# Performance work log

Hardware: AMD Instinct MI355X
Metric: run time of the kernel (lower is better)

The kernel has to match this reference:

```python
import jax, jax.numpy as jnp
import numpy as np

B, S, D, H = 2, 2048, 1024, 16
HD = D // H
FF = 4 * D
EPS = 1e-5


def _ln(x, g, b):
    mu = jnp.mean(x, axis=-1, keepdims=True)
    var = jnp.var(x, axis=-1, keepdims=True)
    return (x - mu) * jax.lax.rsqrt(var + EPS) * g + b


def setup_inputs() -> dict:
    key = jax.random.key(0)
    ks = jax.random.split(key, 8)
    std = 0.02
    inp = {
        'x': jax.random.normal(ks[0], (B, S, D), jnp.float32),
        'mask': jnp.ones((B, S), jnp.int32),
        'Wq': jax.random.normal(ks[1], (D, D), jnp.float32) * std,
        'bq': jnp.zeros((D,), jnp.float32),
        'Wk': jax.random.normal(ks[2], (D, D), jnp.float32) * std,
        'bk': jnp.zeros((D,), jnp.float32),
        'Wv': jax.random.normal(ks[3], (D, D), jnp.float32) * std,
        'bv': jnp.zeros((D,), jnp.float32),
        'Wo': jax.random.normal(ks[4], (D, D), jnp.float32) * std,
        'bo': jnp.zeros((D,), jnp.float32),
        'W1': jax.random.normal(ks[5], (D, FF), jnp.float32) * std,
        'b1': jnp.zeros((FF,), jnp.float32),
        'W2': jax.random.normal(ks[6], (FF, D), jnp.float32) * std,
        'b2': jnp.zeros((D,), jnp.float32),
        'g1': jnp.ones((D,), jnp.float32),
        'be1': jnp.zeros((D,), jnp.float32),
        'g2': jnp.ones((D,), jnp.float32),
        'be2': jnp.zeros((D,), jnp.float32),
    }
    return inp


def reference(x, mask, Wq, bq, Wk, bk, Wv, bv, Wo, bo, W1, b1, W2, b2, g1, be1, g2, be2):
    # multi-head attention (dropout in eval mode => identity)
    q = (x @ Wq + bq).reshape(B, S, H, HD).transpose(0, 2, 1, 3)  # [B,H,S,HD]
    k = (x @ Wk + bk).reshape(B, S, H, HD).transpose(0, 2, 1, 3)
    v = (x @ Wv + bv).reshape(B, S, H, HD).transpose(0, 2, 1, 3)
    scores = jnp.einsum('bhqd,bhkd->bhqk', q, k) / jnp.sqrt(jnp.float32(HD))
    m = mask[:, None, None, :]  # [B,1,1,S] broadcast over queries
    scores = jnp.where(m == 0, jnp.float32(-1e9), scores)
    attn = jax.nn.softmax(scores, axis=-1)
    ao = jnp.einsum('bhqk,bhkd->bhqd', attn, v).transpose(0, 2, 1, 3).reshape(B, S, D)
    attn_out = ao @ Wo + bo
    x1 = _ln(x + attn_out, g1, be1)
    ffn = jax.nn.relu(x1 @ W1 + b1) @ W2 + b2
    return _ln(x1 + ffn, g2, be2)
```

## Files before the change

kernel.cpp:

```cpp
#include <hip/hip_runtime.h>
#include <stdint.h>
#include <stddef.h>

#define B_ 2
#define S_ 2048
#define D_ 1024
#define H_ 16
#define HD_ 64
#define FF_ 4096

typedef unsigned short u16;
typedef __attribute__((ext_vector_type(8))) short bf16x8;
typedef __attribute__((ext_vector_type(4))) float f32x4;

__device__ __forceinline__ u16 f2bf(float f) {
  unsigned u = __float_as_uint(f);
  u += 0x7fffu + ((u >> 16) & 1u);
  return (u16)(u >> 16);
}

__device__ __forceinline__ f32x4 mfma16(bf16x8 a, bf16x8 b, f32x4 c) {
  return __builtin_amdgcn_mfma_f32_16x16x32_bf16(a, b, c, 0, 0, 0);
}

__device__ __forceinline__ void gload16(const void* g, void* l) {
  __builtin_amdgcn_global_load_lds(
      (const __attribute__((address_space(1))) void*)g,
      (__attribute__((address_space(3))) void*)l, 16, 0, 0);
}

__global__ __launch_bounds__(256) void cvt_kernel(const float* __restrict__ src,
                                                  u16* __restrict__ dst, int n) {
  int i = (blockIdx.x * 256 + threadIdx.x) * 4;
  if (i >= n) return;
  float4 v = *(const float4*)(src + i);
  ushort4 o = { f2bf(v.x), f2bf(v.y), f2bf(v.z), f2bf(v.w) };
  *(ushort4*)(dst + i) = o;
}

__global__ __launch_bounds__(256) void transpose_cvt_kernel(
    const float* __restrict__ W, u16* __restrict__ WT, int K, int N) {
  __shared__ u16 t[32][33];
  int k0 = blockIdx.x * 32;
  int n0 = blockIdx.y * 32;
  int tid = threadIdx.x;
  int r = tid >> 3;
  int c = (tid & 7) << 2;
  float4 v = *(const float4*)(W + (size_t)(k0 + r) * N + n0 + c);
  t[r][c + 0] = f2bf(v.x); t[r][c + 1] = f2bf(v.y);
  t[r][c + 2] = f2bf(v.z); t[r][c + 3] = f2bf(v.w);
  __syncthreads();
  ushort4 o;
  o.x = t[c + 0][r]; o.y = t[c + 1][r]; o.z = t[c + 2][r]; o.w = t[c + 3][r];
  *(ushort4*)(WT + (size_t)(n0 + r) * K + k0 + c) = o;
}

template <int MODE>
__global__ __launch_bounds__(256) void gemm_bt(
    const u16* __restrict__ A, const u16* __restrict__ BT,
    const float* __restrict__ bias, void* __restrict__ outp,
    int M, int N, int K) {
  __shared__ __align__(16) u16 As[128 * 32];
  __shared__ __align__(16) u16 Bs[128 * 32];
  int tid = threadIdx.x;
  int lane = tid & 63;
  int wave = tid >> 6;
  int quad = lane >> 4;
  int l16 = lane & 15;
  int m0 = blockIdx.x * 128;
  int n0 = blockIdx.y * 128;
  int wm = (wave >> 1) * 64;
  int wn = (wave & 1) * 64;

  f32x4 zero = {0.f, 0.f, 0.f, 0.f};
  f32x4 acc[4][4];
#pragma unroll
  for (int i = 0; i < 4; i++)
#pragma unroll
    for (int j = 0; j < 4; j++) acc[i][j] = zero;

  int c0 = tid, c1 = tid + 256;
  const u16* ga0 = A + (size_t)(m0 + (c0 >> 2)) * K + (c0 & 3) * 8;
  const u16* ga1 = A + (size_t)(m0 + (c1 >> 2)) * K + (c1 & 3) * 8;
  const u16* gb0 = BT + (size_t)(n0 + (c0 >> 2)) * K + (c0 & 3) * 8;
  const u16* gb1 = BT + (size_t)(n0 + (c1 >> 2)) * K + (c1 & 3) * 8;

  for (int k0 = 0; k0 < K; k0 += 32) {
    gload16(ga0 + k0, &As[c0 * 8]);
    gload16(ga1 + k0, &As[c1 * 8]);
    gload16(gb0 + k0, &Bs[c0 * 8]);
    gload16(gb1 + k0, &Bs[c1 * 8]);
    __syncthreads();
    bf16x8 af[4], bfr[4];
#pragma unroll
    for (int i = 0; i < 4; i++)
      af[i] = *(const bf16x8*)&As[(wm + i * 16 + l16) * 32 + quad * 8];
#pragma unroll
    for (int j = 0; j < 4; j++)
      bfr[j] = *(const bf16x8*)&Bs[(wn + j * 16 + l16) * 32 + quad * 8];
#pragma unroll
    for (int i = 0; i < 4; i++)
#pragma unroll
      for (int j = 0; j < 4; j++)
        acc[i][j] = mfma16(af[i], bfr[j], acc[i][j]);
    __syncthreads();
  }

#pragma unroll
  for (int j = 0; j < 4; j++) {
    int gcol = n0 + wn + j * 16 + l16;
    float bv = bias[gcol];
#pragma unroll
    for (int i = 0; i < 4; i++) {
#pragma unroll
      for (int r = 0; r < 4; r++) {
        int grow = m0 + wm + i * 16 + quad * 4 + r;
        float val = acc[i][j][r] + bv;
        ((u16*)outp)[(size_t)grow * N + gcol] = f2bf(val > 0.f ? val : 0.f);
      }
    }
  }
}

__global__ __launch_bounds__(256) void gemm_bt64(
    const u16* __restrict__ A, const u16* __restrict__ BT,
    const float* __restrict__ bias, float* __restrict__ outp,
    int M, int N, int K) {
  __shared__ __align__(16) u16 As[128 * 32];
  __shared__ __align__(16) u16 Bs[64 * 32];
  int tid = threadIdx.x;
  int lane = tid & 63;
  int wave = tid >> 6;
  int quad = lane >> 4;
  int l16 = lane & 15;
  int m0 = blockIdx.x * 128;
  int n0 = blockIdx.y * 64;
  int wm = (wave >> 1) * 64;
  int wn = (wave & 1) * 32;

  f32x4 zero = {0.f, 0.f, 0.f, 0.f};
  f32x4 acc[4][2];
#pragma unroll
  for (int i = 0; i < 4; i++)
#pragma unroll
    for (int j = 0; j < 2; j++) acc[i][j] = zero;

  int c0 = tid, c1 = tid + 256;
  const u16* ga0 = A + (size_t)(m0 + (c0 >> 2)) * K + (c0 & 3) * 8;
  const u16* ga1 = A + (size_t)(m0 + (c1 >> 2)) * K + (c1 & 3) * 8;
  const u16* gb0 = BT + (size_t)(n0 + (tid >> 2)) * K + (tid & 3) * 8;

  for (int k0 = 0; k0 < K; k0 += 32) {
    gload16(ga0 + k0, &As[c0 * 8]);
    gload16(ga1 + k0, &As[c1 * 8]);
    gload16(gb0 + k0, &Bs[tid * 8]);
    __syncthreads();
    bf16x8 af[4], bfr[2];
#pragma unroll
    for (int i = 0; i < 4; i++)
      af[i] = *(const bf16x8*)&As[(wm + i * 16 + l16) * 32 + quad * 8];
#pragma unroll
    for (int j = 0; j < 2; j++)
      bfr[j] = *(const bf16x8*)&Bs[(wn + j * 16 + l16) * 32 + quad * 8];
#pragma unroll
    for (int i = 0; i < 4; i++)
#pragma unroll
      for (int j = 0; j < 2; j++)
        acc[i][j] = mfma16(af[i], bfr[j], acc[i][j]);
    __syncthreads();
  }

#pragma unroll
  for (int j = 0; j < 2; j++) {
    int gcol = n0 + wn + j * 16 + l16;
    float bv = bias[gcol];
#pragma unroll
    for (int i = 0; i < 4; i++) {
#pragma unroll
      for (int r = 0; r < 4; r++) {
        int grow = m0 + wm + i * 16 + quad * 4 + r;
        outp[(size_t)grow * N + gcol] = acc[i][j][r] + bv;
      }
    }
  }
}

__global__ __launch_bounds__(256) void gemm_qkv(
    const u16* __restrict__ A, const u16* __restrict__ BT,
    const float* __restrict__ bq, const float* __restrict__ bk,
    const float* __restrict__ bvp,
    u16* __restrict__ qb, u16* __restrict__ kb, u16* __restrict__ vb) {
  const int K = 1024;
  __shared__ __align__(16) u16 As[128 * 32];
  __shared__ __align__(16) u16 Bs[128 * 32];
  int tid = threadIdx.x;
  int lane = tid & 63;
  int wave = tid >> 6;
  int quad = lane >> 4;
  int l16 = lane & 15;
  int m0 = blockIdx.x * 128;
  int n0 = blockIdx.y * 128;
  int wm = (wave >> 1) * 64;
  int wn = (wave & 1) * 64;

  f32x4 zero = {0.f, 0.f, 0.f, 0.f};
  f32x4 acc[4][4];
#pragma unroll
  for (int i = 0; i < 4; i++)
#pragma unroll
    for (int j = 0; j < 4; j++) acc[i][j] = zero;

  int c0 = tid, c1 = tid + 256;
  const u16* ga0 = A + (size_t)(m0 + (c0 >> 2)) * K + (c0 & 3) * 8;
  const u16* ga1 = A + (size_t)(m0 + (c1 >> 2)) * K + (c1 & 3) * 8;
  const u16* gb0 = BT + (size_t)(n0 + (c0 >> 2)) * K + (c0 & 3) * 8;
  const u16* gb1 = BT + (size_t)(n0 + (c1 >> 2)) * K + (c1 & 3) * 8;

  for (int k0 = 0; k0 < K; k0 += 32) {
    gload16(ga0 + k0, &As[c0 * 8]);
    gload16(ga1 + k0, &As[c1 * 8]);
    gload16(gb0 + k0, &Bs[c0 * 8]);
    gload16(gb1 + k0, &Bs[c1 * 8]);
    __syncthreads();
    bf16x8 af[4], bfr[4];
#pragma unroll
    for (int i = 0; i < 4; i++)
      af[i] = *(const bf16x8*)&As[(wm + i * 16 + l16) * 32 + quad * 8];
#pragma unroll
    for (int j = 0; j < 4; j++)
      bfr[j] = *(const bf16x8*)&Bs[(wn + j * 16 + l16) * 32 + quad * 8];
#pragma unroll
    for (int i = 0; i < 4; i++)
#pragma unroll
      for (int j = 0; j < 4; j++)
        acc[i][j] = mfma16(af[i], bfr[j], acc[i][j]);
    __syncthreads();
  }

  int region = n0 >> 10;
  const float* bias = region == 0 ? bq : (region == 1 ? bk : bvp);
  u16* outp = region == 0 ? qb : (region == 1 ? kb : vb);

#pragma unroll
  for (int j = 0; j < 4; j++) {
    int gcol = (n0 & 1023) + wn + j * 16 + l16;
    float bv = bias[gcol];
    int h = gcol >> 6, hd = gcol & 63;
#pragma unroll
    for (int i = 0; i < 4; i++) {
#pragma unroll
      for (int r = 0; r < 4; r++) {
        int grow = m0 + wm + i * 16 + quad * 4 + r;
        float val = acc[i][j][r] + bv;
        int b = grow >> 11, s = grow & 2047;
        if (region < 2) {
          outp[(((size_t)(b * H_ + h)) * S_ + s) * HD_ + hd] = f2bf(val);
        } else {
          outp[(((size_t)(b * H_ + h)) * HD_ + hd) * S_ + s] = f2bf(val);
        }
      }
    }
  }
}

__global__ __launch_bounds__(256, 4) void attn_kernel(
    const u16* __restrict__ q, const u16* __restrict__ k,
    const u16* __restrict__ vt, const int* __restrict__ mask,
    u16* __restrict__ ao) {
  __shared__ __align__(16) u16 Ks[64 * 72];
  __shared__ __align__(16) u16 Vs[64 * 72];
  __shared__ __align__(16) u16 Ps[4][16 * 72];
  int tid = threadIdx.x;
  int lane = tid & 63;
  int wave = tid >> 6;
  int quad = lane >> 4;
  int l16 = lane & 15;
  int bh = blockIdx.y;
  int b = bh >> 4;
  int h = bh & 15;
  int qrow0 = blockIdx.x * 64 + wave * 16;

  const u16* qh = q + (size_t)bh * S_ * HD_;
  const u16* kh = k + (size_t)bh * S_ * HD_;
  const u16* vh = vt + (size_t)bh * HD_ * S_;

  bf16x8 qf0 = *(const bf16x8*)(qh + (size_t)(qrow0 + l16) * HD_ + quad * 8);
  bf16x8 qf1 = *(const bf16x8*)(qh + (size_t)(qrow0 + l16) * HD_ + 32 + quad * 8);

  int sr = tid >> 3, sc = tid & 7;
  const u16* kg0 = kh + sr * HD_ + sc * 8;
  const u16* kg1 = kh + (sr + 32) * HD_ + sc * 8;
  const u16* vg0 = vh + (size_t)sr * S_ + sc * 8;
  const u16* vg1 = vh + (size_t)(sr + 32) * S_ + sc * 8;
  int so0 = sr * 72 + sc * 8;
  int so1 = (sr + 32) * 72 + sc * 8;
  const int* mrow = mask + b * S_ + l16;

  float l_part[4] = {0.f, 0.f, 0.f, 0.f};
  f32x4 zero = {0.f, 0.f, 0.f, 0.f};
  f32x4 o_acc[4];
#pragma unroll
  for (int c = 0; c < 4; c++) o_acc[c] = zero;

  u16* pw = &Ps[wave][0];
  const float cexp = 0.125f * 1.4426950408889634f;

  for (int kt = 0; kt < S_; kt += 64) {
    bf16x8 kv0 = *(const bf16x8*)(kg0 + (size_t)kt * HD_);
    bf16x8 kv1 = *(const bf16x8*)(kg1 + (size_t)kt * HD_);
    bf16x8 vv0 = *(const bf16x8*)(vg0 + kt);
    bf16x8 vv1 = *(const bf16x8*)(vg1 + kt);
    int mks[4];
#pragma unroll
    for (int kg = 0; kg < 4; kg++) mks[kg] = mrow[kt + kg * 16];

    __syncthreads();
    *(bf16x8*)&Ks[so0] = kv0;
    *(bf16x8*)&Ks[so1] = kv1;
    *(bf16x8*)&Vs[so0] = vv0;
    *(bf16x8*)&Vs[so1] = vv1;
    __syncthreads();

    f32x4 s[4];
#pragma unroll
    for (int kg = 0; kg < 4; kg++) {
      bf16x8 kb0 = *(const bf16x8*)&Ks[(kg * 16 + l16) * 72 + quad * 8];
      bf16x8 kb1 = *(const bf16x8*)&Ks[(kg * 16 + l16) * 72 + 32 + quad * 8];
      f32x4 t0 = mfma16(qf0, kb0, zero);
      s[kg] = mfma16(qf1, kb1, t0);
    }
#pragma unroll
    for (int kg = 0; kg < 4; kg++) {
#pragma unroll
      for (int r = 0; r < 4; r++) {
        float e = exp2f(s[kg][r] * cexp);
        float p = mks[kg] ? e : 0.f;
        l_part[r] += p;
        pw[(quad * 4 + r) * 72 + kg * 16 + l16] = f2bf(p);
      }
    }
    bf16x8 pf0 = *(const bf16x8*)&pw[l16 * 72 + quad * 8];
    bf16x8 pf1 = *(const bf16x8*)&pw[l16 * 72 + 32 + quad * 8];
#pragma unroll
    for (int c = 0; c < 4; c++) {
      bf16x8 vf0 = *(const bf16x8*)&Vs[(c * 16 + l16) * 72 + quad * 8];
      bf16x8 vf1 = *(const bf16x8*)&Vs[(c * 16 + l16) * 72 + 32 + quad * 8];
      o_acc[c] = mfma16(pf0, vf0, o_acc[c]);
      o_acc[c] = mfma16(pf1, vf1, o_acc[c]);
    }
  }

#pragma unroll
  for (int r = 0; r < 4; r++) {
    float s = l_part[r];
#pragma unroll
    for (int off = 1; off < 16; off <<= 1) s += __shfl_xor(s, off);
    float inv = 1.f / s;
    int srow = qrow0 + quad * 4 + r;
#pragma unroll
    for (int c = 0; c < 4; c++) {
      float val = o_acc[c][r] * inv;
      ao[((size_t)(b * S_ + srow)) * D_ + h * HD_ + c * 16 + l16] = f2bf(val);
    }
  }
}

__global__ __launch_bounds__(256) void ln_kernel(
    const float* __restrict__ xa, const float* __restrict__ xadd,
    const float* __restrict__ g, const float* __restrict__ be,
    float* __restrict__ outf, u16* __restrict__ outb) {
  int row = blockIdx.x;
  int tid = threadIdx.x;
  int lane = tid & 63;
  int wv = tid >> 6;
  const float4 a = *(const float4*)(xa + (size_t)row * D_ + tid * 4);
  const float4 c = *(const float4*)(xadd + (size_t)row * D_ + tid * 4);
  float v0 = a.x + c.x, v1 = a.y + c.y, v2 = a.z + c.z, v3 = a.w + c.w;
  float s = v0 + v1 + v2 + v3;
  float sq = v0 * v0 + v1 * v1 + v2 * v2 + v3 * v3;
#pragma unroll
  for (int off = 1; off < 64; off <<= 1) {
    s += __shfl_xor(s, off);
    sq += __shfl_xor(sq, off);
  }
  __shared__ float red[8];
  if (lane == 0) { red[wv] = s; red[4 + wv] = sq; }
  __syncthreads();
  s = red[0] + red[1] + red[2] + red[3];
  sq = red[4] + red[5] + red[6] + red[7];
  float mean = s * (1.f / D_);
  float var = sq * (1.f / D_) - mean * mean;
  float rstd = rsqrtf(var + 1e-5f);
  const float4 gv = *(const float4*)(g + tid * 4);
  const float4 bv = *(const float4*)(be + tid * 4);
  float y0 = (v0 - mean) * rstd * gv.x + bv.x;
  float y1 = (v1 - mean) * rstd * gv.y + bv.y;
  float y2 = (v2 - mean) * rstd * gv.z + bv.z;
  float y3 = (v3 - mean) * rstd * gv.w + bv.w;
  float4 o = {y0, y1, y2, y3};
  *(float4*)(outf + (size_t)row * D_ + tid * 4) = o;
  if (outb) {
    ushort4 ob = {f2bf(y0), f2bf(y1), f2bf(y2), f2bf(y3)};
    *(ushort4*)(outb + (size_t)row * D_ + tid * 4) = ob;
  }
}

extern "C" void kernel_launch(void* const* d_in, const int* in_sizes, int n_in,
                              void* d_out, int out_size, void* d_ws, size_t ws_size,
                              hipStream_t stream) {
  const float* x = (const float*)d_in[0];
  const int* mask = (const int*)d_in[1];
  const float* Wq = (const float*)d_in[2];
  const float* bq = (const float*)d_in[3];
  const float* Wk = (const float*)d_in[4];
  const float* bk = (const float*)d_in[5];
  const float* Wv = (const float*)d_in[6];
  const float* bv = (const float*)d_in[7];
  const float* Wo = (const float*)d_in[8];
  const float* bo = (const float*)d_in[9];
  const float* W1 = (const float*)d_in[10];
  const float* b1 = (const float*)d_in[11];
  const float* W2 = (const float*)d_in[12];
  const float* b2 = (const float*)d_in[13];
  const float* g1 = (const float*)d_in[14];
  const float* be1 = (const float*)d_in[15];
  const float* g2 = (const float*)d_in[16];
  const float* be2 = (const float*)d_in[17];

  const size_t MB = 1ull << 20;
  char* ws = (char*)d_ws;
  u16* wTq = (u16*)(ws + 0 * MB);
  u16* wTk = (u16*)(ws + 2 * MB);
  u16* wTv = (u16*)(ws + 4 * MB);
  u16* wTo = (u16*)(ws + 6 * MB);
  u16* w1T = (u16*)(ws + 8 * MB);
  u16* w2T = (u16*)(ws + 16 * MB);
  u16* xb  = (u16*)(ws + 24 * MB);
  u16* qb  = (u16*)(ws + 32 * MB);
  u16* kb  = (u16*)(ws + 40 * MB);
  u16* vb  = (u16*)(ws + 48 * MB);
  u16* ao  = (u16*)(ws + 56 * MB);
  float* proj = (float*)(ws + 64 * MB);
  float* x1f  = (float*)(ws + 24 * MB);
  u16*   x1b  = (u16*)(ws + 40 * MB);
  u16*   h1   = (u16*)(ws + 48 * MB);
  float* ffn2 = (float*)(ws + 80 * MB);

  cvt_kernel<<<dim3((B_ * S_ * D_) / 1024), dim3(256), 0, stream>>>(x, xb, B_ * S_ * D_);
  transpose_cvt_kernel<<<dim3(32, 32), dim3(256), 0, stream>>>(Wq, wTq, D_, D_);
  transpose_cvt_kernel<<<dim3(32, 32), dim3(256), 0, stream>>>(Wk, wTk, D_, D_);
  transpose_cvt_kernel<<<dim3(32, 32), dim3(256), 0, stream>>>(Wv, wTv, D_, D_);
  transpose_cvt_kernel<<<dim3(32, 32), dim3(256), 0, stream>>>(Wo, wTo, D_, D_);
  transpose_cvt_kernel<<<dim3(32, 128), dim3(256), 0, stream>>>(W1, w1T, D_, FF_);
  transpose_cvt_kernel<<<dim3(128, 32), dim3(256), 0, stream>>>(W2, w2T, FF_, D_);

  gemm_qkv<<<dim3(32, 24), dim3(256), 0, stream>>>(xb, wTq, bq, bk, bv, qb, kb, vb);

  attn_kernel<<<dim3(S_ / 64, B_ * H_), dim3(256), 0, stream>>>(qb, kb, vb, mask, ao);

  gemm_bt64<<<dim3(32, 16), dim3(256), 0, stream>>>(ao, wTo, bo, proj, 4096, 1024, 1024);

  ln_kernel<<<dim3(4096), dim3(256), 0, stream>>>(x, proj, g1, be1, x1f, x1b);

  gemm_bt<3><<<dim3(32, 32), dim3(256), 0, stream>>>(x1b, w1T, b1, h1, 4096, 4096, 1024);
  gemm_bt64<<<dim3(32, 16), dim3(256), 0, stream>>>(h1, w2T, b2, ffn2, 4096, 1024, 4096);

  ln_kernel<<<dim3(4096), dim3(256), 0, stream>>>(x1f, ffn2, g2, be2, (float*)d_out, (u16*)nullptr);
}
```

Before: 431.8 us.

## Use split-K 128x128 GEMMs for output projections, fold softmax scale into Q

The Wo and W2 GEMMs change from 128x64 tiles to 128x128 tiles with a 2-way split-K. Each half writes its own fp32 partial buffer, and the LayerNorm kernel sums both partials with the residual. This raises data reuse per tile while keeping the block count, in exchange for more fp32 partial-buffer traffic. The softmax scale times log2(e) is now applied in the QKV epilogue, so the attention loop skips a per-element multiply. Attention also permutes the K rows in shared memory so that two adjacent probabilities can be packed into one 32-bit store, and the mask is read as int2.

```diff
diff --git a/kernel.cpp b/kernel.cpp
--- a/kernel.cpp
+++ b/kernel.cpp
@@ -55,10 +55,9 @@
   *(ushort4*)(WT + (size_t)(n0 + r) * K + k0 + c) = o;
 }
 
-template <int MODE>
-__global__ __launch_bounds__(256) void gemm_bt(
+__global__ __launch_bounds__(256) void gemm_bt_relu(
     const u16* __restrict__ A, const u16* __restrict__ BT,
-    const float* __restrict__ bias, void* __restrict__ outp,
+    const float* __restrict__ bias, u16* __restrict__ outp,
     int M, int N, int K) {
   __shared__ __align__(16) u16 As[128 * 32];
   __shared__ __align__(16) u16 Bs[128 * 32];
@@ -116,70 +115,75 @@
       for (int r = 0; r < 4; r++) {
         int grow = m0 + wm + i * 16 + quad * 4 + r;
         float val = acc[i][j][r] + bv;
-        ((u16*)outp)[(size_t)grow * N + gcol] = f2bf(val > 0.f ? val : 0.f);
-      }
-    }
-  }
-}
-
-__global__ __launch_bounds__(256) void gemm_bt64(
+        outp[(size_t)grow * N + gcol] = f2bf(val > 0.f ? val : 0.f);
+      }
+    }
+  }
+}
+
+__global__ __launch_bounds__(256) void gemm_bt_sk2(
     const u16* __restrict__ A, const u16* __restrict__ BT,
     const float* __restrict__ bias, float* __restrict__ outp,
-    int M, int N, int K) {
+    int M, int N, int K, int Kc) {
   __shared__ __align__(16) u16 As[128 * 32];
-  __shared__ __align__(16) u16 Bs[64 * 32];
+  __shared__ __align__(16) u16 Bs[128 * 32];
   int tid = threadIdx.x;
   int lane = tid & 63;
   int wave = tid >> 6;
   int quad = lane >> 4;
   int l16 = lane & 15;
   int m0 = blockIdx.x * 128;
-  int n0 = blockIdx.y * 64;
+  int n0 = blockIdx.y * 128;
+  int kb = blockIdx.z * Kc;
   int wm = (wave >> 1) * 64;
-  int wn = (wave & 1) * 32;
+  int wn = (wave & 1) * 64;
 
   f32x4 zero = {0.f, 0.f, 0.f, 0.f};
-  f32x4 acc[4][2];
+  f32x4 acc[4][4];
 #pragma unroll
   for (int i = 0; i < 4; i++)
 #pragma unroll
-    for (int j = 0; j < 2; j++) acc[i][j] = zero;
+    for (int j = 0; j < 4; j++) acc[i][j] = zero;
 
   int c0 = tid, c1 = tid + 256;
-  const u16* ga0 = A + (size_t)(m0 + (c0 >> 2)) * K + (c0 & 3) * 8;
-  const u16* ga1 = A + (size_t)(m0 + (c1 >> 2)) * K + (c1 & 3) * 8;
-  const u16* gb0 = BT + (size_t)(n0 + (tid >> 2)) * K + (tid & 3) * 8;
-
-  for (int k0 = 0; k0 < K; k0 += 32) {
+  const u16* ga0 = A + (size_t)(m0 + (c0 >> 2)) * K + (c0 & 3) * 8 + kb;
+  const u16* ga1 = A + (size_t)(m0 + (c1 >> 2)) * K + (c1 & 3) * 8 + kb;
+  const u16* gb0 = BT + (size_t)(n0 + (c0 >> 2)) * K + (c0 & 3) * 8 + kb;
+  const u16* gb1 = BT + (size_t)(n0 + (c1 >> 2)) * K + (c1 & 3) * 8 + kb;
+
+  for (int k0 = 0; k0 < Kc; k0 += 32) {
     gload16(ga0 + k0, &As[c0 * 8]);
     gload16(ga1 + k0, &As[c1 * 8]);
-    gload16(gb0 + k0, &Bs[tid * 8]);
-    __syncthreads();
-    bf16x8 af[4], bfr[2];
+    gload16(gb0 + k0, &Bs[c0 * 8]);
+    gload16(gb1 + k0, &Bs[c1 * 8]);
+    __syncthreads();
+    bf16x8 af[4], bfr[4];
 #pragma unroll
     for (int i = 0; i < 4; i++)
       af[i] = *(const bf16x8*)&As[(wm + i * 16 + l16) * 32 + quad * 8];
 #pragma unroll
-    for (int j = 0; j < 2; j++)
+    for (int j = 0; j < 4; j++)
       bfr[j] = *(const bf16x8*)&Bs[(wn + j * 16 + l16) * 32 + quad * 8];
 #pragma unroll
     for (int i = 0; i < 4; i++)
 #pragma unroll
-      for (int j = 0; j < 2; j++)
+      for (int j = 0; j < 4; j++)
         acc[i][j] = mfma16(af[i], bfr[j], acc[i][j]);
     __syncthreads();
   }
 
-#pragma unroll
-  for (int j = 0; j < 2; j++) {
+  float* outz = outp + (size_t)blockIdx.z * M * N;
+  float biasmul = (blockIdx.z == 0) ? 1.f : 0.f;
+#pragma unroll
+  for (int j = 0; j < 4; j++) {
     int gcol = n0 + wn + j * 16 + l16;
-    float bv = bias[gcol];
+    float bv = bias[gcol] * biasmul;
 #pragma unroll
     for (int i = 0; i < 4; i++) {
 #pragma unroll
       for (int r = 0; r < 4; r++) {
         int grow = m0 + wm + i * 16 + quad * 4 + r;
-        outp[(size_t)grow * N + gcol] = acc[i][j][r] + bv;
+        outz[(size_t)grow * N + gcol] = acc[i][j][r] + bv;
       }
     }
   }
@@ -240,6 +244,7 @@
   int region = n0 >> 10;
   const float* bias = region == 0 ? bq : (region == 1 ? bk : bvp);
   u16* outp = region == 0 ? qb : (region == 1 ? kb : vb);
+  float scale = region == 0 ? 0.125f * 1.4426950408889634f : 1.f;
 
 #pragma unroll
   for (int j = 0; j < 4; j++) {
@@ -251,7 +256,7 @@
 #pragma unroll
       for (int r = 0; r < 4; r++) {
         int grow = m0 + wm + i * 16 + quad * 4 + r;
-        float val = acc[i][j][r] + bv;
+        float val = (acc[i][j][r] + bv) * scale;
         int b = grow >> 11, s = grow & 2047;
         if (region < 2) {
           outp[(((size_t)(b * H_ + h)) * S_ + s) * HD_ + hd] = f2bf(val);
@@ -292,9 +297,12 @@
   const u16* kg1 = kh + (sr + 32) * HD_ + sc * 8;
   const u16* vg0 = vh + (size_t)sr * S_ + sc * 8;
   const u16* vg1 = vh + (size_t)(sr + 32) * S_ + sc * 8;
-  int so0 = sr * 72 + sc * 8;
-  int so1 = (sr + 32) * 72 + sc * 8;
-  const int* mrow = mask + b * S_ + l16;
+  int kr0 = (sr & 1) * 16 + (sr >> 1);
+  int ko0 = kr0 * 72 + sc * 8;
+  int ko1 = (32 + kr0) * 72 + sc * 8;
+  int vo0 = sr * 72 + sc * 8;
+  int vo1 = (sr + 32) * 72 + sc * 8;
+  const int* mrow = mask + b * S_ + 2 * l16;
 
   float l_part[4] = {0.f, 0.f, 0.f, 0.f};
   f32x4 zero = {0.f, 0.f, 0.f, 0.f};
@@ -303,40 +311,48 @@
   for (int c = 0; c < 4; c++) o_acc[c] = zero;
 
   u16* pw = &Ps[wave][0];
-  const float cexp = 0.125f * 1.4426950408889634f;
 
   for (int kt = 0; kt < S_; kt += 64) {
     bf16x8 kv0 = *(const bf16x8*)(kg0 + (size_t)kt * HD_);
     bf16x8 kv1 = *(const bf16x8*)(kg1 + (size_t)kt * HD_);
     bf16x8 vv0 = *(const bf16x8*)(vg0 + kt);
     bf16x8 vv1 = *(const bf16x8*)(vg1 + kt);
-    int mks[4];
-#pragma unroll
-    for (int kg = 0; kg < 4; kg++) mks[kg] = mrow[kt + kg * 16];
-
-    __syncthreads();
-    *(bf16x8*)&Ks[so0] = kv0;
-    *(bf16x8*)&Ks[so1] = kv1;
-    *(bf16x8*)&Vs[so0] = vv0;
-    *(bf16x8*)&Vs[so1] = vv1;
-    __syncthreads();
-
-    f32x4 s[4];
-#pragma unroll
-    for (int kg = 0; kg < 4; kg++) {
-      bf16x8 kb0 = *(const bf16x8*)&Ks[(kg * 16 + l16) * 72 + quad * 8];
-      bf16x8 kb1 = *(const bf16x8*)&Ks[(kg * 16 + l16) * 72 + 32 + quad * 8];
-      f32x4 t0 = mfma16(qf0, kb0, zero);
-      s[kg] = mfma16(qf1, kb1, t0);
-    }
-#pragma unroll
-    for (int kg = 0; kg < 4; kg++) {
+    int2 mk0 = *(const int2*)(mrow + kt);
+    int2 mk1 = *(const int2*)(mrow + kt + 32);
+
+    __syncthreads();
+    *(bf16x8*)&Ks[ko0] = kv0;
+    *(bf16x8*)&Ks[ko1] = kv1;
+    *(bf16x8*)&Vs[vo0] = vv0;
+    *(bf16x8*)&Vs[vo1] = vv1;
+    __syncthreads();
+
+#pragma unroll
+    for (int g = 0; g < 2; g++) {
+      int2 mk = g == 0 ? mk0 : mk1;
+      f32x4 se, so;
+      {
+        int rowb = (g * 32 + l16) * 72;
+        bf16x8 e0 = *(const bf16x8*)&Ks[rowb + quad * 8];
+        bf16x8 e1 = *(const bf16x8*)&Ks[rowb + 32 + quad * 8];
+        se = mfma16(qf1, e1, mfma16(qf0, e0, zero));
+      }
+      {
+        int rowb = (g * 32 + 16 + l16) * 72;
+        bf16x8 o0 = *(const bf16x8*)&Ks[rowb + quad * 8];
+        bf16x8 o1 = *(const bf16x8*)&Ks[rowb + 32 + quad * 8];
+        so = mfma16(qf1, o1, mfma16(qf0, o0, zero));
+      }
 #pragma unroll
       for (int r = 0; r < 4; r++) {
-        float e = exp2f(s[kg][r] * cexp);
-        float p = mks[kg] ? e : 0.f;
-        l_part[r] += p;
-        pw[(quad * 4 + r) * 72 + kg * 16 + l16] = f2bf(p);
+        float e0 = exp2f(se[r]);
+        float e1 = exp2f(so[r]);
+        float p0 = mk.x ? e0 : 0.f;
+        float p1 = mk.y ? e1 : 0.f;
+        l_part[r] += p0 + p1;
+        unsigned pk = __builtin_amdgcn_perm(__float_as_uint(p1),
+                                            __float_as_uint(p0), 0x07060302u);
+        *(unsigned*)&pw[(quad * 4 + r) * 72 + g * 32 + 2 * l16] = pk;
       }
     }
     bf16x8 pf0 = *(const bf16x8*)&pw[l16 * 72 + quad * 8];
@@ -366,7 +382,8 @@
 }
 
 __global__ __launch_bounds__(256) void ln_kernel(
-    const float* __restrict__ xa, const float* __restrict__ xadd,
+    const float* __restrict__ xa, const float* __restrict__ add0,
+    const float* __restrict__ add1,
     const float* __restrict__ g, const float* __restrict__ be,
     float* __restrict__ outf, u16* __restrict__ outb) {
   int row = blockIdx.x;
@@ -374,8 +391,10 @@
   int lane = tid & 63;
   int wv = tid >> 6;
   const float4 a = *(const float4*)(xa + (size_t)row * D_ + tid * 4);
-  const float4 c = *(const float4*)(xadd + (size_t)row * D_ + tid * 4);
-  float v0 = a.x + c.x, v1 = a.y + c.y, v2 = a.z + c.z, v3 = a.w + c.w;
+  const float4 c = *(const float4*)(add0 + (size_t)row * D_ + tid * 4);
+  const float4 d = *(const float4*)(add1 + (size_t)row * D_ + tid * 4);
+  float v0 = a.x + c.x + d.x, v1 = a.y + c.y + d.y;
+  float v2 = a.z + c.z + d.z, v3 = a.w + c.w + d.w;
   float s = v0 + v1 + v2 + v3;
   float sq = v0 * v0 + v1 * v1 + v2 * v2 + v3 * v3;
 #pragma unroll
@@ -443,8 +462,8 @@
   float* proj = (float*)(ws + 64 * MB);
   float* x1f  = (float*)(ws + 24 * MB);
   u16*   x1b  = (u16*)(ws + 40 * MB);
-  u16*   h1   = (u16*)(ws + 48 * MB);
-  float* ffn2 = (float*)(ws + 80 * MB);
+  u16*   h1   = (u16*)(ws + 96 * MB);
+  float* ffn2 = (float*)(ws + 48 * MB);
 
   cvt_kernel<<<dim3((B_ * S_ * D_) / 1024), dim3(256), 0, stream>>>(x, xb, B_ * S_ * D_);
   transpose_cvt_kernel<<<dim3(32, 32), dim3(256), 0, stream>>>(Wq, wTq, D_, D_);
@@ -458,12 +477,15 @@
 
   attn_kernel<<<dim3(S_ / 64, B_ * H_), dim3(256), 0, stream>>>(qb, kb, vb, mask, ao);
 
-  gemm_bt64<<<dim3(32, 16), dim3(256), 0, stream>>>(ao, wTo, bo, proj, 4096, 1024, 1024);
-
-  ln_kernel<<<dim3(4096), dim3(256), 0, stream>>>(x, proj, g1, be1, x1f, x1b);
-
-  gemm_bt<3><<<dim3(32, 32), dim3(256), 0, stream>>>(x1b, w1T, b1, h1, 4096, 4096, 1024);
-  gemm_bt64<<<dim3(32, 16), dim3(256), 0, stream>>>(h1, w2T, b2, ffn2, 4096, 1024, 4096);
-
-  ln_kernel<<<dim3(4096), dim3(256), 0, stream>>>(x1f, ffn2, g2, be2, (float*)d_out, (u16*)nullptr);
-}
+  gemm_bt_sk2<<<dim3(32, 8, 2), dim3(256), 0, stream>>>(ao, wTo, bo, proj, 4096, 1024, 1024, 512);
+
+  ln_kernel<<<dim3(4096), dim3(256), 0, stream>>>(
+      x, proj, proj + (size_t)4096 * 1024, g1, be1, x1f, x1b);
+
+  gemm_bt_relu<<<dim3(32, 32), dim3(256), 0, stream>>>(x1b, w1T, b1, h1, 4096, 4096, 1024);
+
+  gemm_bt_sk2<<<dim3(32, 8, 2), dim3(256), 0, stream>>>(h1, w2T, b2, ffn2, 4096, 1024, 4096, 2048);
+
+  ln_kernel<<<dim3(4096), dim3(256), 0, stream>>>(
+      x1f, ffn2, ffn2 + (size_t)4096 * 1024, g2, be2, (float*)d_out, (u16*)nullptr);
+}
```

New measurement: 406.9 us. 1.06x faster.
